# Performance work log

Measured on AMD Instinct MI355X. Metric: run time of the kernel, lower is better.

The kernel has to match this reference:

```python
import jax, jax.numpy as jnp
import numpy as np

B, T, I, H, L = 32768, 30, 4, 64, 32


def _lstm_layer(x, Wih, Whh, bih, bhh):
    """PyTorch-semantics single-layer LSTM, batch_first. Returns (outputs [B,T,H], h_T [B,H])."""
    # Precompute input contribution for all timesteps: [B, T, 4H]
    xg = jnp.einsum('bti,gi->btg', x, Wih) + bih + bhh
    Hh = Whh.shape[1]
    h0 = jnp.zeros((x.shape[0], Hh), x.dtype)

    def step(carry, xg_t):
        h, c = carry
        g = xg_t + h @ Whh.T  # [B, 4H]
        i, f, gg, o = jnp.split(g, 4, axis=-1)  # PyTorch gate order i,f,g,o
        c = jax.nn.sigmoid(f) * c + jax.nn.sigmoid(i) * jnp.tanh(gg)
        h = jax.nn.sigmoid(o) * jnp.tanh(c)
        return (h, c), h

    (hT, _), hs = jax.lax.scan(step, (h0, h0), jnp.swapaxes(xg, 0, 1))
    return jnp.swapaxes(hs, 0, 1), hT


def setup_inputs() -> dict:
    key = jax.random.key(0)
    ks = jax.random.split(key, 20)
    s = 0.1  # weight scale for numerical stability
    inp = {
        'x': jax.random.normal(ks[0], (B, T, I), jnp.float32),
        'enc1_Wih': s * jax.random.normal(ks[1], (4 * H, I), jnp.float32),
        'enc1_Whh': s * jax.random.normal(ks[2], (4 * H, H), jnp.float32),
        'enc1_bih': s * jax.random.normal(ks[3], (4 * H,), jnp.float32),
        'enc1_bhh': s * jax.random.normal(ks[4], (4 * H,), jnp.float32),
        'enc2_Wih': s * jax.random.normal(ks[5], (4 * L, H), jnp.float32),
        'enc2_Whh': s * jax.random.normal(ks[6], (4 * L, L), jnp.float32),
        'enc2_bih': s * jax.random.normal(ks[7], (4 * L,), jnp.float32),
        'enc2_bhh': s * jax.random.normal(ks[8], (4 * L,), jnp.float32),
        'dec1_Wih': s * jax.random.normal(ks[9], (4 * H, L), jnp.float32),
        'dec1_Whh': s * jax.random.normal(ks[10], (4 * H, H), jnp.float32),
        'dec1_bih': s * jax.random.normal(ks[11], (4 * H,), jnp.float32),
        'dec1_bhh': s * jax.random.normal(ks[12], (4 * H,), jnp.float32),
        'dec2_Wih': s * jax.random.normal(ks[13], (4 * I, H), jnp.float32),
        'dec2_Whh': s * jax.random.normal(ks[14], (4 * I, I), jnp.float32),
        'dec2_bih': s * jax.random.normal(ks[15], (4 * I,), jnp.float32),
        'dec2_bhh': s * jax.random.normal(ks[16], (4 * I,), jnp.float32),
    }
    return inp


def reference(x, enc1_Wih, enc1_Whh, enc1_bih, enc1_bhh,
              enc2_Wih, enc2_Whh, enc2_bih, enc2_bhh,
              dec1_Wih, dec1_Whh, dec1_bih, dec1_bhh,
              dec2_Wih, dec2_Whh, dec2_bih, dec2_bhh):
    seq_len = x.shape[1]
    out, _ = _lstm_layer(x, enc1_Wih, enc1_Whh, enc1_bih, enc1_bhh)
    out, h = _lstm_layer(out, enc2_Wih, enc2_Whh, enc2_bih, enc2_bhh)
    latent = jnp.repeat(h[:, None, :], seq_len, axis=1)  # [B, T, L]
    out, _ = _lstm_layer(latent, dec1_Wih, dec1_Whh, dec1_bih, dec1_bhh)
    out, _ = _lstm_layer(out, dec2_Wih, dec2_Whh, dec2_bih, dec2_bhh)
    return out
```

## Files before the change

### kernel.cpp

```cpp
#include <hip/hip_runtime.h>
#include <stdint.h>


typedef unsigned short u16;
typedef unsigned int u32;
typedef __attribute__((ext_vector_type(8))) short bf16x8;
typedef __attribute__((ext_vector_type(4))) short s16x4;
typedef __attribute__((ext_vector_type(4))) float f32x4;

#define BATCH 32768
#define TT 30
#define IN 4
#define WAVES 8
#define BLOCKT (WAVES * 64)
#define MB 16
#define BPB (WAVES * MB)

#define WREG 18432
#define O_WHH1HI 0
#define O_W1FOLD 8192
#define O_WIH2HI 12288
#define O_WHH2HI 16384
#define O_WHH3HI 0
#define O_WIH3HI 8192
#define O_WIH4HI 12288
#define O_W4HHF  12800

#define NBIAS 400
#define BUFW 1344
#define SMEM_WORDS (WREG + NBIAS + WAVES * BUFW)
#define SMEM_BYTES (SMEM_WORDS * 4)

#define WB() __builtin_amdgcn_wave_barrier()
#define MFMA(a, b, c) __builtin_amdgcn_mfma_f32_16x16x32_bf16((a), (b), (c), 0, 0, 0)

__device__ __forceinline__ u16 f2bf(float f) {
    u32 u = __float_as_uint(f);
    u += 0x7fffu + ((u >> 16) & 1u);
    return (u16)(u >> 16);
}
__device__ __forceinline__ float bf2f(u16 v) { return __uint_as_float(((u32)v) << 16); }
__device__ __forceinline__ float sigf(float x) {
    return __builtin_amdgcn_rcpf(1.f + __expf(-x));
}
__device__ __forceinline__ float tanh_(float x) {
    const float t = __expf(2.f * x);
    return fmaf(-2.f, __builtin_amdgcn_rcpf(t + 1.f), 1.f);
}

template <int KT>
__device__ __forceinline__ void stageBh(u16* hi, const float* src, int N, int tid) {
    const int K = KT * 32;
    const int total = N * K;
    for (int idx = tid; idx < total; idx += BLOCKT) {
        const int j = idx & 7;
        const int l = (idx >> 3) & 63;
        const int pair = idx >> 9;
        const int kt = pair & (KT - 1);
        const int nt = pair / KT;
        const int n = (nt << 4) | (l & 15);
        const int k = (kt << 5) + ((l >> 4) << 3) + j;
        hi[idx] = f2bf(src[n * K + k]);
    }
}

__device__ __forceinline__ f32x4 splat4(float b) {
    f32x4 v = {b, b, b, b};
    return v;
}

__global__ __launch_bounds__(BLOCKT, 2) void lstm_ae(
    const float* __restrict__ x,
    const float* __restrict__ w1ih, const float* __restrict__ w1hh,
    const float* __restrict__ b1i, const float* __restrict__ b1h,
    const float* __restrict__ w2ih, const float* __restrict__ w2hh,
    const float* __restrict__ b2i, const float* __restrict__ b2h,
    const float* __restrict__ w3ih, const float* __restrict__ w3hh,
    const float* __restrict__ b3i, const float* __restrict__ b3h,
    const float* __restrict__ w4ih, const float* __restrict__ w4hh,
    const float* __restrict__ b4i, const float* __restrict__ b4h,
    float* __restrict__ out) {
    extern __shared__ float smem[];
    float* W = smem;
    float* biasF = smem + WREG;
    float* bufs = biasF + NBIAS;

    const int tid = threadIdx.x;
    const int wave = tid >> 6, lane = tid & 63;
    const int col = lane & 15, quad = lane >> 4;

    float* wbuf = bufs + wave * BUFW;
    u16* h1hi = (u16*)(wbuf);
    u16* xfold = (u16*)(wbuf + 512);
    u16* h2hi = (u16*)(wbuf + 768);
    float* gbuf = wbuf + 1024;
    float* bufH4 = wbuf + 1280;

    const int b0w = blockIdx.x * BPB + wave * MB;

    stageBh<2>((u16*)(W + O_WHH1HI), w1hh, 256, tid);
    stageBh<2>((u16*)(W + O_WIH2HI), w2ih, 128, tid);
    stageBh<1>((u16*)(W + O_WHH2HI), w2hh, 128, tid);
    {
        u16* F = (u16*)(W + O_W1FOLD);
        for (int idx = tid; idx < 16 * 512; idx += BLOCKT) {
            const int nt = idx >> 9;
            const int rem = idx & 511;
            const int l = rem >> 3;
            const int j = rem & 7;
            const int q = l >> 4;
            const int n = (nt << 4) | (l & 15);
            u16 v = 0;
            if (q == 0) {
                v = f2bf(w1ih[n * 4 + (j & 3)]);
            } else if (q == 1) {
                if (j < 4) {
                    const float w = w1ih[n * 4 + j];
                    v = f2bf(w - bf2f(f2bf(w)));
                } else if (j == 4) {
                    v = f2bf(b1i[n] + b1h[n]);
                } else if (j == 5) {
                    const float b = b1i[n] + b1h[n];
                    v = f2bf(b - bf2f(f2bf(b)));
                }
            }
            F[idx] = v;
        }
    }
    for (int i = tid; i < 128; i += BLOCKT) biasF[i] = b2i[i] + b2h[i];
    for (int i = tid; i < 256; i += BLOCKT) biasF[128 + i] = b3i[i] + b3h[i];
    for (int i = tid; i < 16; i += BLOCKT) biasF[384 + i] = b4i[i] + b4h[i];
    {
        u32* z = (u32*)wbuf;
        for (int i = lane; i < BUFW; i += 64) z[i] = 0u;
    }
    WB();
    if (quad == 1) {
        xfold[lane * 8 + 4] = (u16)0x3F80;
        xfold[lane * 8 + 5] = (u16)0x3F80;
    }
    __syncthreads();

    float bias2r[8];
#pragma unroll
    for (int nt = 0; nt < 8; ++nt) bias2r[nt] = biasF[nt * 16 + col];
    const float bias4r = biasF[384 + col];

    const u16* Whh1hi = (const u16*)(W + O_WHH1HI);
    const u16* W1fold = (const u16*)(W + O_W1FOLD);
    const u16* Wih2hi = (const u16*)(W + O_WIH2HI);
    const u16* Whh2hi = (const u16*)(W + O_WHH2HI);

    float c1[4][4], c2[2][4];
#pragma unroll
    for (int q = 0; q < 4; ++q)
#pragma unroll
        for (int r = 0; r < 4; ++r) c1[q][r] = 0.f;
#pragma unroll
    for (int q = 0; q < 2; ++q)
#pragma unroll
        for (int r = 0; r < 4; ++r) c2[q][r] = 0.f;

    const f32x4 zf = {0.f, 0.f, 0.f, 0.f};
    float4 xcur = *reinterpret_cast<const float4*>(
        x + ((size_t)(b0w + col) * TT + 0) * IN);

    for (int t = 0; t < TT; ++t) {
        {
            const u16 xh0 = f2bf(xcur.x), xh1 = f2bf(xcur.y);
            const u16 xh2 = f2bf(xcur.z), xh3 = f2bf(xcur.w);
            if (quad == 0) {
                bf16x8 v;
                v[0] = (short)xh0; v[1] = (short)xh1; v[2] = (short)xh2; v[3] = (short)xh3;
                v[4] = (short)f2bf(xcur.x - bf2f(xh0));
                v[5] = (short)f2bf(xcur.y - bf2f(xh1));
                v[6] = (short)f2bf(xcur.z - bf2f(xh2));
                v[7] = (short)f2bf(xcur.w - bf2f(xh3));
                *reinterpret_cast<bf16x8*>(xfold + lane * 8) = v;
            } else if (quad == 1) {
                s16x4 v;
                v[0] = (short)xh0; v[1] = (short)xh1; v[2] = (short)xh2; v[3] = (short)xh3;
                *reinterpret_cast<s16x4*>(xfold + lane * 8) = v;
            }
        }
        WB();
        {
            const int tn = (t + 1 < TT) ? t + 1 : t;
            xcur = *reinterpret_cast<const float4*>(
                x + ((size_t)(b0w + col) * TT + tn) * IN);
        }
        bf16x8 a1h0 = *reinterpret_cast<const bf16x8*>(h1hi + lane * 8);
        bf16x8 a1h1 = *reinterpret_cast<const bf16x8*>(h1hi + (64 + lane) * 8);
        const bf16x8 a1x = *reinterpret_cast<const bf16x8*>(xfold + lane * 8);
        f32x4 acc1[16];
#pragma unroll
        for (int nt = 0; nt < 16; ++nt) {
            const bf16x8 bx = *reinterpret_cast<const bf16x8*>(W1fold + (nt * 64 + lane) * 8);
            const bf16x8 bh0 = *reinterpret_cast<const bf16x8*>(Whh1hi + ((nt * 2 + 0) * 64 + lane) * 8);
            const bf16x8 bh1 = *reinterpret_cast<const bf16x8*>(Whh1hi + ((nt * 2 + 1) * 64 + lane) * 8);
            f32x4 a = MFMA(a1x, bx, zf);
            a = MFMA(a1h0, bh0, a);
            a = MFMA(a1h1, bh1, a);
            acc1[nt] = a;
        }
        WB();
#pragma unroll
        for (int q = 0; q < 4; ++q) {
            const int kt = q >> 1;
            const int lup = ((((q & 1) << 1) + (col >> 3)) << 4);
            const int j = col & 7;
#pragma unroll
            for (int r = 0; r < 4; ++r) {
                const int m = quad * 4 + r;
                const float iv = sigf(acc1[q][r]);
                const float fv = sigf(acc1[4 + q][r]);
                const float gv = tanh_(acc1[8 + q][r]);
                const float ov = sigf(acc1[12 + q][r]);
                c1[q][r] = fv * c1[q][r] + iv * gv;
                const float h = ov * tanh_(c1[q][r]);
                h1hi[(kt * 64 + m + lup) * 8 + j] = f2bf(h);
            }
        }
        WB();
        a1h0 = *reinterpret_cast<const bf16x8*>(h1hi + lane * 8);
        a1h1 = *reinterpret_cast<const bf16x8*>(h1hi + (64 + lane) * 8);
        const bf16x8 a2h = *reinterpret_cast<const bf16x8*>(h2hi + lane * 8);
        f32x4 acc2[8];
#pragma unroll
        for (int nt = 0; nt < 8; ++nt) {
            const bf16x8 bh0 = *reinterpret_cast<const bf16x8*>(Wih2hi + ((nt * 2 + 0) * 64 + lane) * 8);
            const bf16x8 bh1 = *reinterpret_cast<const bf16x8*>(Wih2hi + ((nt * 2 + 1) * 64 + lane) * 8);
            const bf16x8 ch = *reinterpret_cast<const bf16x8*>(Whh2hi + (nt * 64 + lane) * 8);
            f32x4 a = splat4(bias2r[nt]);
            a = MFMA(a1h0, bh0, a);
            a = MFMA(a1h1, bh1, a);
            a = MFMA(a2h, ch, a);
            acc2[nt] = a;
        }
        WB();
#pragma unroll
        for (int q = 0; q < 2; ++q) {
            const int lup = (((q << 1) + (col >> 3)) << 4);
            const int j = col & 7;
#pragma unroll
            for (int r = 0; r < 4; ++r) {
                const int m = quad * 4 + r;
                const float iv = sigf(acc2[q][r]);
                const float fv = sigf(acc2[2 + q][r]);
                const float gv = tanh_(acc2[4 + q][r]);
                const float ov = sigf(acc2[6 + q][r]);
                c2[q][r] = fv * c2[q][r] + iv * gv;
                const float h = ov * tanh_(c2[q][r]);
                h2hi[(m + lup) * 8 + j] = f2bf(h);
            }
        }
        WB();
    }

    __syncthreads();

    stageBh<2>((u16*)(W + O_WHH3HI), w3hh, 256, tid);
    stageBh<1>((u16*)(W + O_WIH3HI), w3ih, 256, tid);
    stageBh<2>((u16*)(W + O_WIH4HI), w4ih, 16, tid);
    for (int i = tid; i < 64; i += BLOCKT) W[O_W4HHF + i] = w4hh[i];
    {
        u32* z = (u32*)wbuf;
        for (int i = lane; i < 512; i += 64) z[i] = 0u;
        if (lane < 64) bufH4[lane] = 0.f;
    }
    __syncthreads();

    const u16* Whh3hi = (const u16*)(W + O_WHH3HI);
    const u16* Wih3hi = (const u16*)(W + O_WIH3HI);
    const u16* Wih4hi = (const u16*)(W + O_WIH4HI);
    const float* W4hhF = W + O_W4HHF;

    f32x4 preactL[16];
    {
        const bf16x8 aLh = *reinterpret_cast<const bf16x8*>(h2hi + lane * 8);
#pragma unroll
        for (int nt = 0; nt < 16; ++nt) {
            const bf16x8 bh = *reinterpret_cast<const bf16x8*>(Wih3hi + (nt * 64 + lane) * 8);
            preactL[nt] = MFMA(aLh, bh, splat4(biasF[128 + nt * 16 + col]));
        }
    }

    float c3[4][4], c4 = 0.f;
#pragma unroll
    for (int q = 0; q < 4; ++q)
#pragma unroll
        for (int r = 0; r < 4; ++r) c3[q][r] = 0.f;
    const int u4 = lane & 3, mb = lane >> 2;

    for (int t = 0; t < TT; ++t) {
        bf16x8 a3h0 = *reinterpret_cast<const bf16x8*>(h1hi + lane * 8);
        bf16x8 a3h1 = *reinterpret_cast<const bf16x8*>(h1hi + (64 + lane) * 8);
        f32x4 acc3[16];
#pragma unroll
        for (int nt = 0; nt < 16; ++nt) {
            const bf16x8 bh0 = *reinterpret_cast<const bf16x8*>(Whh3hi + ((nt * 2 + 0) * 64 + lane) * 8);
            const bf16x8 bh1 = *reinterpret_cast<const bf16x8*>(Whh3hi + ((nt * 2 + 1) * 64 + lane) * 8);
            f32x4 a = MFMA(a3h0, bh0, preactL[nt]);
            a = MFMA(a3h1, bh1, a);
            acc3[nt] = a;
        }
        WB();
#pragma unroll
        for (int q = 0; q < 4; ++q) {
            const int kt = q >> 1;
            const int lup = ((((q & 1) << 1) + (col >> 3)) << 4);
            const int j = col & 7;
#pragma unroll
            for (int r = 0; r < 4; ++r) {
                const int m = quad * 4 + r;
                const float iv = sigf(acc3[q][r]);
                const float fv = sigf(acc3[4 + q][r]);
                const float gv = tanh_(acc3[8 + q][r]);
                const float ov = sigf(acc3[12 + q][r]);
                c3[q][r] = fv * c3[q][r] + iv * gv;
                const float h = ov * tanh_(c3[q][r]);
                h1hi[(kt * 64 + m + lup) * 8 + j] = f2bf(h);
            }
        }
        WB();
        a3h0 = *reinterpret_cast<const bf16x8*>(h1hi + lane * 8);
        a3h1 = *reinterpret_cast<const bf16x8*>(h1hi + (64 + lane) * 8);
        f32x4 acc4 = splat4(bias4r);
        {
            const float4 w4 = *reinterpret_cast<const float4*>(W4hhF + col * 4);
#pragma unroll
            for (int r = 0; r < 4; ++r) {
                const float4 hv = *reinterpret_cast<const float4*>(bufH4 + (quad * 4 + r) * 4);
                float s = acc4[r];
                s = fmaf(w4.x, hv.x, s);
                s = fmaf(w4.y, hv.y, s);
                s = fmaf(w4.z, hv.z, s);
                s = fmaf(w4.w, hv.w, s);
                acc4[r] = s;
            }
        }
        {
            const bf16x8 bh0 = *reinterpret_cast<const bf16x8*>(Wih4hi + (0 * 64 + lane) * 8);
            const bf16x8 bh1 = *reinterpret_cast<const bf16x8*>(Wih4hi + (1 * 64 + lane) * 8);
            acc4 = MFMA(a3h0, bh0, acc4);
            acc4 = MFMA(a3h1, bh1, acc4);
        }
        WB();
#pragma unroll
        for (int r = 0; r < 4; ++r) gbuf[(quad * 4 + r) * 16 + col] = acc4[r];
        WB();
        {
            const float iv = sigf(gbuf[mb * 16 + u4]);
            const float fv = sigf(gbuf[mb * 16 + 4 + u4]);
            const float gv = tanh_(gbuf[mb * 16 + 8 + u4]);
            const float ov = sigf(gbuf[mb * 16 + 12 + u4]);
            c4 = fv * c4 + iv * gv;
            const float h = ov * tanh_(c4);
            out[((size_t)(b0w + mb) * TT + t) * IN + u4] = h;
            bufH4[mb * 4 + u4] = h;
        }
        WB();
    }
}

extern "C" void kernel_launch(void* const* d_in, const int* in_sizes, int n_in,
                              void* d_out, int out_size, void* d_ws, size_t ws_size,
                              hipStream_t stream) {
    (void)in_sizes; (void)n_in; (void)d_ws; (void)ws_size; (void)out_size;
    hipFuncSetAttribute(reinterpret_cast<const void*>(lstm_ae),
                        hipFuncAttributeMaxDynamicSharedMemorySize, SMEM_BYTES);
    const float* xi = (const float*)d_in[0];
    const float* w1ih = (const float*)d_in[1];
    const float* w1hh = (const float*)d_in[2];
    const float* b1i = (const float*)d_in[3];
    const float* b1h = (const float*)d_in[4];
    const float* w2ih = (const float*)d_in[5];
    const float* w2hh = (const float*)d_in[6];
    const float* b2i = (const float*)d_in[7];
    const float* b2h = (const float*)d_in[8];
    const float* w3ih = (const float*)d_in[9];
    const float* w3hh = (const float*)d_in[10];
    const float* b3i = (const float*)d_in[11];
    const float* b3h = (const float*)d_in[12];
    const float* w4ih = (const float*)d_in[13];
    const float* w4hh = (const float*)d_in[14];
    const float* b4i = (const float*)d_in[15];
    const float* b4h = (const float*)d_in[16];
    float* out = (float*)d_out;

    lstm_ae<<<dim3(BATCH / BPB), dim3(BLOCKT), SMEM_BYTES, stream>>>(
        xi, w1ih, w1hh, b1i, b1h, w2ih, w2hh, b2i, b2h,
        w3ih, w3hh, b3i, b3h, w4ih, w4hh, b4i, b4h, out);
}
```

Measured before the change: 340.9 us.

## Split layers across wave pairs with double-buffered hidden state pipelining

Each block now has 16 waves arranged as 8 pairs. Within a pair, one wave runs layer 1 (and later layer 3) at step s while the other runs layer 2 (and later layer 4) at step s-1. A double-buffered h1 tile hands data between them, with a block-wide __syncthreads every step. The intent is to overlap the two stacked layers of each encoder/decoder stage instead of running them serially in one wave. In exchange it adds a block barrier per step, an extra pipeline step, and idle time on the lighter layer-2/4 waves. The layer-3 latent projection is also recomputed inside the loop rather than precomputed.

```diff
diff --git a/kernel.cpp b/kernel.cpp
--- a/kernel.cpp
+++ b/kernel.cpp
@@ -11,10 +11,11 @@
 #define BATCH 32768
 #define TT 30
 #define IN 4
-#define WAVES 8
+#define WAVES 16
 #define BLOCKT (WAVES * 64)
 #define MB 16
-#define BPB (WAVES * MB)
+#define NPAIR 8
+#define BPB (NPAIR * MB)
 
 #define WREG 18432
 #define O_WHH1HI 0
@@ -27,8 +28,8 @@
 #define O_W4HHF  12800
 
 #define NBIAS 400
-#define BUFW 1344
-#define SMEM_WORDS (WREG + NBIAS + WAVES * BUFW)
+#define PBUF 1600
+#define SMEM_WORDS (WREG + NBIAS + NPAIR * PBUF)
 #define SMEM_BYTES (SMEM_WORDS * 4)
 
 #define WB() __builtin_amdgcn_wave_barrier()
@@ -69,7 +70,7 @@
     return v;
 }
 
-__global__ __launch_bounds__(BLOCKT, 2) void lstm_ae(
+__global__ __launch_bounds__(BLOCKT, 4) void lstm_ae(
     const float* __restrict__ x,
     const float* __restrict__ w1ih, const float* __restrict__ w1hh,
     const float* __restrict__ b1i, const float* __restrict__ b1h,
@@ -87,16 +88,17 @@
 
     const int tid = threadIdx.x;
     const int wave = tid >> 6, lane = tid & 63;
+    const int pair = wave & 7, role = wave >> 3;
     const int col = lane & 15, quad = lane >> 4;
 
-    float* wbuf = bufs + wave * BUFW;
-    u16* h1hi = (u16*)(wbuf);
-    u16* xfold = (u16*)(wbuf + 512);
-    u16* h2hi = (u16*)(wbuf + 768);
-    float* gbuf = wbuf + 1024;
-    float* bufH4 = wbuf + 1280;
-
-    const int b0w = blockIdx.x * BPB + wave * MB;
+    float* pb = bufs + pair * PBUF;
+    u16* h1d = (u16*)pb;
+    u16* h2b = (u16*)(pb + 1024);
+    u16* xfold = (u16*)(pb + 1280);
+    float* gbuf = pb + 1280;
+    float* bufH4 = pb + 1536;
+
+    const int b0w = blockIdx.x * BPB + pair * MB;
 
     stageBh<2>((u16*)(W + O_WHH1HI), w1hh, 256, tid);
     stageBh<2>((u16*)(W + O_WIH2HI), w2ih, 128, tid);
@@ -131,27 +133,29 @@
     for (int i = tid; i < 256; i += BLOCKT) biasF[128 + i] = b3i[i] + b3h[i];
     for (int i = tid; i < 16; i += BLOCKT) biasF[384 + i] = b4i[i] + b4h[i];
     {
-        u32* z = (u32*)wbuf;
-        for (int i = lane; i < BUFW; i += 64) z[i] = 0u;
+        u32* z = (u32*)pb;
+        if (role == 0) {
+            for (int i = lane; i < 1024; i += 64) z[i] = 0u;
+            for (int i = lane; i < 256; i += 64) z[1280 + i] = 0u;
+        } else {
+            for (int i = lane; i < 256; i += 64) z[1024 + i] = 0u;
+            if (lane < 64) bufH4[lane] = 0.f;
+        }
     }
     WB();
-    if (quad == 1) {
+    if (role == 0 && quad == 1) {
         xfold[lane * 8 + 4] = (u16)0x3F80;
         xfold[lane * 8 + 5] = (u16)0x3F80;
     }
     __syncthreads();
-
-    float bias2r[8];
-#pragma unroll
-    for (int nt = 0; nt < 8; ++nt) bias2r[nt] = biasF[nt * 16 + col];
-    const float bias4r = biasF[384 + col];
 
     const u16* Whh1hi = (const u16*)(W + O_WHH1HI);
     const u16* W1fold = (const u16*)(W + O_W1FOLD);
     const u16* Wih2hi = (const u16*)(W + O_WIH2HI);
     const u16* Whh2hi = (const u16*)(W + O_WHH2HI);
 
-    float c1[4][4], c2[2][4];
+    float c1[4][4];
+    float c2[2][4];
 #pragma unroll
     for (int q = 0; q < 4; ++q)
 #pragma unroll
@@ -160,112 +164,129 @@
     for (int q = 0; q < 2; ++q)
 #pragma unroll
         for (int r = 0; r < 4; ++r) c2[q][r] = 0.f;
+    float bias2r[8];
+#pragma unroll
+    for (int nt = 0; nt < 8; ++nt) bias2r[nt] = biasF[nt * 16 + col];
 
     const f32x4 zf = {0.f, 0.f, 0.f, 0.f};
-    float4 xcur = *reinterpret_cast<const float4*>(
-        x + ((size_t)(b0w + col) * TT + 0) * IN);
-
-    for (int t = 0; t < TT; ++t) {
-        {
-            const u16 xh0 = f2bf(xcur.x), xh1 = f2bf(xcur.y);
-            const u16 xh2 = f2bf(xcur.z), xh3 = f2bf(xcur.w);
-            if (quad == 0) {
-                bf16x8 v;
-                v[0] = (short)xh0; v[1] = (short)xh1; v[2] = (short)xh2; v[3] = (short)xh3;
-                v[4] = (short)f2bf(xcur.x - bf2f(xh0));
-                v[5] = (short)f2bf(xcur.y - bf2f(xh1));
-                v[6] = (short)f2bf(xcur.z - bf2f(xh2));
-                v[7] = (short)f2bf(xcur.w - bf2f(xh3));
-                *reinterpret_cast<bf16x8*>(xfold + lane * 8) = v;
-            } else if (quad == 1) {
-                s16x4 v;
-                v[0] = (short)xh0; v[1] = (short)xh1; v[2] = (short)xh2; v[3] = (short)xh3;
-                *reinterpret_cast<s16x4*>(xfold + lane * 8) = v;
+    float4 xcur;
+    if (role == 0)
+        xcur = *reinterpret_cast<const float4*>(x + ((size_t)(b0w + col) * TT + 0) * IN);
+
+    for (int s = 0; s <= TT; ++s) {
+        if (role == 0) {
+            if (s < TT) {
+                {
+                    const u16 xh0 = f2bf(xcur.x), xh1 = f2bf(xcur.y);
+                    const u16 xh2 = f2bf(xcur.z), xh3 = f2bf(xcur.w);
+                    if (quad == 0) {
+                        bf16x8 v;
+                        v[0] = (short)xh0; v[1] = (short)xh1; v[2] = (short)xh2; v[3] = (short)xh3;
+                        v[4] = (short)f2bf(xcur.x - bf2f(xh0));
+                        v[5] = (short)f2bf(xcur.y - bf2f(xh1));
+                        v[6] = (short)f2bf(xcur.z - bf2f(xh2));
+                        v[7] = (short)f2bf(xcur.w - bf2f(xh3));
+                        *reinterpret_cast<bf16x8*>(xfold + lane * 8) = v;
+                    } else if (quad == 1) {
+                        s16x4 v;
+                        v[0] = (short)xh0; v[1] = (short)xh1; v[2] = (short)xh2; v[3] = (short)xh3;
+                        *reinterpret_cast<s16x4*>(xfold + lane * 8) = v;
+                    }
+                }
+                WB();
+                {
+                    const int tn = (s + 1 < TT) ? s + 1 : s;
+                    xcur = *reinterpret_cast<const float4*>(
+                        x + ((size_t)(b0w + col) * TT + tn) * IN);
+                }
+                const u16* hprev = h1d + (((s + 1) & 1) << 10);
+                u16* hout = h1d + ((s & 1) << 10);
+                const bf16x8 a1h0 = *reinterpret_cast<const bf16x8*>(hprev + lane * 8);
+                const bf16x8 a1h1 = *reinterpret_cast<const bf16x8*>(hprev + (64 + lane) * 8);
+                const bf16x8 a1x = *reinterpret_cast<const bf16x8*>(xfold + lane * 8);
+#pragma unroll
+                for (int half = 0; half < 2; ++half) {
+                    f32x4 acc[8];
+#pragma unroll
+                    for (int i = 0; i < 8; ++i) {
+                        const int q = half * 2 + (i >> 2);
+                        const int nt = (i & 3) * 4 + q;
+                        const bf16x8 bx = *reinterpret_cast<const bf16x8*>(W1fold + (nt * 64 + lane) * 8);
+                        const bf16x8 bh0 = *reinterpret_cast<const bf16x8*>(Whh1hi + ((nt * 2 + 0) * 64 + lane) * 8);
+                        const bf16x8 bh1 = *reinterpret_cast<const bf16x8*>(Whh1hi + ((nt * 2 + 1) * 64 + lane) * 8);
+                        f32x4 a = MFMA(a1x, bx, zf);
+                        a = MFMA(a1h0, bh0, a);
+                        a = MFMA(a1h1, bh1, a);
+                        acc[i] = a;
+                    }
+#pragma unroll
+                    for (int qi = 0; qi < 2; ++qi) {
+                        const int q = half * 2 + qi;
+                        const int kt = q >> 1;
+                        const int lup = ((((q & 1) << 1) + (col >> 3)) << 4);
+                        const int j = col & 7;
+#pragma unroll
+                        for (int r = 0; r < 4; ++r) {
+                            const int m = quad * 4 + r;
+                            const float iv = sigf(acc[qi * 4 + 0][r]);
+                            const float fv = sigf(acc[qi * 4 + 1][r]);
+                            const float gv = tanh_(acc[qi * 4 + 2][r]);
+                            const float ov = sigf(acc[qi * 4 + 3][r]);
+                            c1[q][r] = fv * c1[q][r] + iv * gv;
+                            const float h = ov * tanh_(c1[q][r]);
+                            hout[(kt * 64 + m + lup) * 8 + j] = f2bf(h);
+                        }
+                    }
+                }
+            }
+        } else {
+            if (s >= 1) {
+                const u16* hprev = h1d + (((s + 1) & 1) << 10);
+                const bf16x8 a1h0 = *reinterpret_cast<const bf16x8*>(hprev + lane * 8);
+                const bf16x8 a1h1 = *reinterpret_cast<const bf16x8*>(hprev + (64 + lane) * 8);
+                const bf16x8 a2h = *reinterpret_cast<const bf16x8*>(h2b + lane * 8);
+                f32x4 acc2[8];
+#pragma unroll
+                for (int nt = 0; nt < 8; ++nt) {
+                    const bf16x8 bh0 = *reinterpret_cast<const bf16x8*>(Wih2hi + ((nt * 2 + 0) * 64 + lane) * 8);
+                    const bf16x8 bh1 = *reinterpret_cast<const bf16x8*>(Wih2hi + ((nt * 2 + 1) * 64 + lane) * 8);
+                    const bf16x8 ch = *reinterpret_cast<const bf16x8*>(Whh2hi + (nt * 64 + lane) * 8);
+                    f32x4 a = splat4(bias2r[nt]);
+                    a = MFMA(a1h0, bh0, a);
+                    a = MFMA(a1h1, bh1, a);
+                    a = MFMA(a2h, ch, a);
+                    acc2[nt] = a;
+                }
+                WB();
+#pragma unroll
+                for (int q = 0; q < 2; ++q) {
+                    const int lup = (((q << 1) + (col >> 3)) << 4);
+                    const int j = col & 7;
+#pragma unroll
+                    for (int r = 0; r < 4; ++r) {
+                        const int m = quad * 4 + r;
+                        const float iv = sigf(acc2[q][r]);
+                        const float fv = sigf(acc2[2 + q][r]);
+                        const float gv = tanh_(acc2[4 + q][r]);
+                        const float ov = sigf(acc2[6 + q][r]);
+                        c2[q][r] = fv * c2[q][r] + iv * gv;
+                        const float h = ov * tanh_(c2[q][r]);
+                        h2b[(m + lup) * 8 + j] = f2bf(h);
+                    }
+                }
             }
         }
-        WB();
-        {
-            const int tn = (t + 1 < TT) ? t + 1 : t;
-            xcur = *reinterpret_cast<const float4*>(
-                x + ((size_t)(b0w + col) * TT + tn) * IN);
-        }
-        bf16x8 a1h0 = *reinterpret_cast<const bf16x8*>(h1hi + lane * 8);
-        bf16x8 a1h1 = *reinterpret_cast<const bf16x8*>(h1hi + (64 + lane) * 8);
-        const bf16x8 a1x = *reinterpret_cast<const bf16x8*>(xfold + lane * 8);
-        f32x4 acc1[16];
-#pragma unroll
-        for (int nt = 0; nt < 16; ++nt) {
-            const bf16x8 bx = *reinterpret_cast<const bf16x8*>(W1fold + (nt * 64 + lane) * 8);
-            const bf16x8 bh0 = *reinterpret_cast<const bf16x8*>(Whh1hi + ((nt * 2 + 0) * 64 + lane) * 8);
-            const bf16x8 bh1 = *reinterpret_cast<const bf16x8*>(Whh1hi + ((nt * 2 + 1) * 64 + lane) * 8);
-            f32x4 a = MFMA(a1x, bx, zf);
-            a = MFMA(a1h0, bh0, a);
-            a = MFMA(a1h1, bh1, a);
-            acc1[nt] = a;
-        }
-        WB();
-#pragma unroll
-        for (int q = 0; q < 4; ++q) {
-            const int kt = q >> 1;
-            const int lup = ((((q & 1) << 1) + (col >> 3)) << 4);
-            const int j = col & 7;
-#pragma unroll
-            for (int r = 0; r < 4; ++r) {
-                const int m = quad * 4 + r;
-                const float iv = sigf(acc1[q][r]);
-                const float fv = sigf(acc1[4 + q][r]);
-                const float gv = tanh_(acc1[8 + q][r]);
-                const float ov = sigf(acc1[12 + q][r]);
-                c1[q][r] = fv * c1[q][r] + iv * gv;
-                const float h = ov * tanh_(c1[q][r]);
-                h1hi[(kt * 64 + m + lup) * 8 + j] = f2bf(h);
-            }
-        }
-        WB();
-        a1h0 = *reinterpret_cast<const bf16x8*>(h1hi + lane * 8);
-        a1h1 = *reinterpret_cast<const bf16x8*>(h1hi + (64 + lane) * 8);
-        const bf16x8 a2h = *reinterpret_cast<const bf16x8*>(h2hi + lane * 8);
-        f32x4 acc2[8];
-#pragma unroll
-        for (int nt = 0; nt < 8; ++nt) {
-            const bf16x8 bh0 = *reinterpret_cast<const bf16x8*>(Wih2hi + ((nt * 2 + 0) * 64 + lane) * 8);
-            const bf16x8 bh1 = *reinterpret_cast<const bf16x8*>(Wih2hi + ((nt * 2 + 1) * 64 + lane) * 8);
-            const bf16x8 ch = *reinterpret_cast<const bf16x8*>(Whh2hi + (nt * 64 + lane) * 8);
-            f32x4 a = splat4(bias2r[nt]);
-            a = MFMA(a1h0, bh0, a);
-            a = MFMA(a1h1, bh1, a);
-            a = MFMA(a2h, ch, a);
-            acc2[nt] = a;
-        }
-        WB();
-#pragma unroll
-        for (int q = 0; q < 2; ++q) {
-            const int lup = (((q << 1) + (col >> 3)) << 4);
-            const int j = col & 7;
-#pragma unroll
-            for (int r = 0; r < 4; ++r) {
-                const int m = quad * 4 + r;
-                const float iv = sigf(acc2[q][r]);
-                const float fv = sigf(acc2[2 + q][r]);
-                const float gv = tanh_(acc2[4 + q][r]);
-                const float ov = sigf(acc2[6 + q][r]);
-                c2[q][r] = fv * c2[q][r] + iv * gv;
-                const float h = ov * tanh_(c2[q][r]);
-                h2hi[(m + lup) * 8 + j] = f2bf(h);
-            }
-        }
-        WB();
-    }
-
-    __syncthreads();
+        __syncthreads();
+    }
 
     stageBh<2>((u16*)(W + O_WHH3HI), w3hh, 256, tid);
     stageBh<1>((u16*)(W + O_WIH3HI), w3ih, 256, tid);
     stageBh<2>((u16*)(W + O_WIH4HI), w4ih, 16, tid);
     for (int i = tid; i < 64; i += BLOCKT) W[O_W4HHF + i] = w4hh[i];
-    {
-        u32* z = (u32*)wbuf;
-        for (int i = lane; i < 512; i += 64) z[i] = 0u;
+    if (role == 0) {
+        u32* z = (u32*)pb;
+        for (int i = lane; i < 1024; i += 64) z[i] = 0u;
+    } else {
         if (lane < 64) bufH4[lane] = 0.f;
     }
     __syncthreads();
@@ -275,91 +296,108 @@
     const u16* Wih4hi = (const u16*)(W + O_WIH4HI);
     const float* W4hhF = W + O_W4HHF;
 
-    f32x4 preactL[16];
-    {
-        const bf16x8 aLh = *reinterpret_cast<const bf16x8*>(h2hi + lane * 8);
-#pragma unroll
-        for (int nt = 0; nt < 16; ++nt) {
-            const bf16x8 bh = *reinterpret_cast<const bf16x8*>(Wih3hi + (nt * 64 + lane) * 8);
-            preactL[nt] = MFMA(aLh, bh, splat4(biasF[128 + nt * 16 + col]));
-        }
-    }
-
-    float c3[4][4], c4 = 0.f;
-#pragma unroll
-    for (int q = 0; q < 4; ++q)
-#pragma unroll
-        for (int r = 0; r < 4; ++r) c3[q][r] = 0.f;
+    float c3[4][4], bias3r[16];
+    float c4 = 0.f, bias4r = 0.f;
+    bf16x8 aLh;
+    if (role == 0) {
+#pragma unroll
+        for (int q = 0; q < 4; ++q)
+#pragma unroll
+            for (int r = 0; r < 4; ++r) c3[q][r] = 0.f;
+#pragma unroll
+        for (int nt = 0; nt < 16; ++nt) bias3r[nt] = biasF[128 + nt * 16 + col];
+        aLh = *reinterpret_cast<const bf16x8*>(h2b + lane * 8);
+    } else {
+        bias4r = biasF[384 + col];
+    }
     const int u4 = lane & 3, mb = lane >> 2;
 
-    for (int t = 0; t < TT; ++t) {
-        bf16x8 a3h0 = *reinterpret_cast<const bf16x8*>(h1hi + lane * 8);
-        bf16x8 a3h1 = *reinterpret_cast<const bf16x8*>(h1hi + (64 + lane) * 8);
-        f32x4 acc3[16];
-#pragma unroll
-        for (int nt = 0; nt < 16; ++nt) {
-            const bf16x8 bh0 = *reinterpret_cast<const bf16x8*>(Whh3hi + ((nt * 2 + 0) * 64 + lane) * 8);
-            const bf16x8 bh1 = *reinterpret_cast<const bf16x8*>(Whh3hi + ((nt * 2 + 1) * 64 + lane) * 8);
-            f32x4 a = MFMA(a3h0, bh0, preactL[nt]);
-            a = MFMA(a3h1, bh1, a);
-            acc3[nt] = a;
-        }
-        WB();
-#pragma unroll
-        for (int q = 0; q < 4; ++q) {
-            const int kt = q >> 1;
-            const int lup = ((((q & 1) << 1) + (col >> 3)) << 4);
-            const int j = col & 7;
-#pragma unroll
-            for (int r = 0; r < 4; ++r) {
-                const int m = quad * 4 + r;
-                const float iv = sigf(acc3[q][r]);
-                const float fv = sigf(acc3[4 + q][r]);
-                const float gv = tanh_(acc3[8 + q][r]);
-                const float ov = sigf(acc3[12 + q][r]);
-                c3[q][r] = fv * c3[q][r] + iv * gv;
-                const float h = ov * tanh_(c3[q][r]);
-                h1hi[(kt * 64 + m + lup) * 8 + j] = f2bf(h);
+    for (int s = 0; s <= TT; ++s) {
+        if (role == 0) {
+            if (s < TT) {
+                const u16* hprev = h1d + (((s + 1) & 1) << 10);
+                u16* hout = h1d + ((s & 1) << 10);
+                const bf16x8 a3h0 = *reinterpret_cast<const bf16x8*>(hprev + lane * 8);
+                const bf16x8 a3h1 = *reinterpret_cast<const bf16x8*>(hprev + (64 + lane) * 8);
+#pragma unroll
+                for (int half = 0; half < 2; ++half) {
+                    f32x4 acc[8];
+#pragma unroll
+                    for (int i = 0; i < 8; ++i) {
+                        const int q = half * 2 + (i >> 2);
+                        const int nt = (i & 3) * 4 + q;
+                        const bf16x8 bL = *reinterpret_cast<const bf16x8*>(Wih3hi + (nt * 64 + lane) * 8);
+                        const bf16x8 bh0 = *reinterpret_cast<const bf16x8*>(Whh3hi + ((nt * 2 + 0) * 64 + lane) * 8);
+                        const bf16x8 bh1 = *reinterpret_cast<const bf16x8*>(Whh3hi + ((nt * 2 + 1) * 64 + lane) * 8);
+                        f32x4 a = MFMA(aLh, bL, splat4(bias3r[nt]));
+                        a = MFMA(a3h0, bh0, a);
+                        a = MFMA(a3h1, bh1, a);
+                        acc[i] = a;
+                    }
+#pragma unroll
+                    for (int qi = 0; qi < 2; ++qi) {
+                        const int q = half * 2 + qi;
+                        const int kt = q >> 1;
+                        const int lup = ((((q & 1) << 1) + (col >> 3)) << 4);
+                        const int j = col & 7;
+#pragma unroll
+                        for (int r = 0; r < 4; ++r) {
+                            const int m = quad * 4 + r;
+                            const float iv = sigf(acc[qi * 4 + 0][r]);
+                            const float fv = sigf(acc[qi * 4 + 1][r]);
+                            const float gv = tanh_(acc[qi * 4 + 2][r]);
+                            const float ov = sigf(acc[qi * 4 + 3][r]);
+                            c3[q][r] = fv * c3[q][r] + iv * gv;
+                            const float h = ov * tanh_(c3[q][r]);
+                            hout[(kt * 64 + m + lup) * 8 + j] = f2bf(h);
+                        }
+                    }
+                }
+            }
+        } else {
+            if (s >= 1) {
+                const int t = s - 1;
+                const u16* hprev = h1d + (((s + 1) & 1) << 10);
+                const bf16x8 a3h0 = *reinterpret_cast<const bf16x8*>(hprev + lane * 8);
+                const bf16x8 a3h1 = *reinterpret_cast<const bf16x8*>(hprev + (64 + lane) * 8);
+                f32x4 acc4 = splat4(bias4r);
+                {
+                    const float4 w4 = *reinterpret_cast<const float4*>(W4hhF + col * 4);
+#pragma unroll
+                    for (int r = 0; r < 4; ++r) {
+                        const float4 hv = *reinterpret_cast<const float4*>(bufH4 + (quad * 4 + r) * 4);
+                        float sa = acc4[r];
+                        sa = fmaf(w4.x, hv.x, sa);
+                        sa = fmaf(w4.y, hv.y, sa);
+                        sa = fmaf(w4.z, hv.z, sa);
+                        sa = fmaf(w4.w, hv.w, sa);
+                        acc4[r] = sa;
+                    }
+                }
+                {
+                    const bf16x8 bh0 = *reinterpret_cast<const bf16x8*>(Wih4hi + (0 * 64 + lane) * 8);
+                    const bf16x8 bh1 = *reinterpret_cast<const bf16x8*>(Wih4hi + (1 * 64 + lane) * 8);
+                    acc4 = MFMA(a3h0, bh0, acc4);
+                    acc4 = MFMA(a3h1, bh1, acc4);
+                }
+                WB();
+#pragma unroll
+                for (int r = 0; r < 4; ++r) gbuf[(quad * 4 + r) * 16 + col] = acc4[r];
+                WB();
+                {
+                    const float iv = sigf(gbuf[mb * 16 + u4]);
+                    const float fv = sigf(gbuf[mb * 16 + 4 + u4]);
+                    const float gv = tanh_(gbuf[mb * 16 + 8 + u4]);
+                    const float ov = sigf(gbuf[mb * 16 + 12 + u4]);
+                    c4 = fv * c4 + iv * gv;
+                    const float h = ov * tanh_(c4);
+                    out[((size_t)(b0w + mb) * TT + t) * IN + u4] = h;
+                    bufH4[mb * 4 + u4] = h;
+                }
+                WB();
             }
         }
-        WB();
-        a3h0 = *reinterpret_cast<const bf16x8*>(h1hi + lane * 8);
-        a3h1 = *reinterpret_cast<const bf16x8*>(h1hi + (64 + lane) * 8);
-        f32x4 acc4 = splat4(bias4r);
-        {
-            const float4 w4 = *reinterpret_cast<const float4*>(W4hhF + col * 4);
-#pragma unroll
-            for (int r = 0; r < 4; ++r) {
-                const float4 hv = *reinterpret_cast<const float4*>(bufH4 + (quad * 4 + r) * 4);
-                float s = acc4[r];
-                s = fmaf(w4.x, hv.x, s);
-                s = fmaf(w4.y, hv.y, s);
-                s = fmaf(w4.z, hv.z, s);
-                s = fmaf(w4.w, hv.w, s);
-                acc4[r] = s;
-            }
-        }
-        {
-            const bf16x8 bh0 = *reinterpret_cast<const bf16x8*>(Wih4hi + (0 * 64 + lane) * 8);
-            const bf16x8 bh1 = *reinterpret_cast<const bf16x8*>(Wih4hi + (1 * 64 + lane) * 8);
-            acc4 = MFMA(a3h0, bh0, acc4);
-            acc4 = MFMA(a3h1, bh1, acc4);
-        }
-        WB();
-#pragma unroll
-        for (int r = 0; r < 4; ++r) gbuf[(quad * 4 + r) * 16 + col] = acc4[r];
-        WB();
-        {
-            const float iv = sigf(gbuf[mb * 16 + u4]);
-            const float fv = sigf(gbuf[mb * 16 + 4 + u4]);
-            const float gv = tanh_(gbuf[mb * 16 + 8 + u4]);
-            const float ov = sigf(gbuf[mb * 16 + 12 + u4]);
-            c4 = fv * c4 + iv * gv;
-            const float h = ov * tanh_(c4);
-            out[((size_t)(b0w + mb) * TT + t) * IN + u4] = h;
-            bufH4[mb * 4 + u4] = h;
-        }
-        WB();
+        __syncthreads();
     }
 }
 
```

Measured after the change: 428.5 us. +25.7%, slower.
